# Performance work log

Measured on AMD Instinct MI355X. Metric: run time of the kernel, lower is better.

## Reference

```python
import jax, jax.numpy as jnp
import numpy as np

GROUP_SIZES = (64, 128, 256, 96, 160, 224, 192, 288, 320, 112, 80, 48, 32, 16, 32)
LENGTH = 512
ALPHABET = 21


def setup_inputs() -> dict:
    key = jax.random.key(0)
    keys = jax.random.split(key, len(GROUP_SIZES) + 1)
    n_samples = int(sum(GROUP_SIZES))
    inp = {"x": jax.random.normal(keys[0], (n_samples, LENGTH, ALPHABET), dtype=jnp.float32)}
    for i, g in enumerate(GROUP_SIZES):
        inp[f"mat{i}"] = jax.random.normal(keys[i + 1], (g, g), dtype=jnp.float32)
    return inp


def reference(x, mat0, mat1, mat2, mat3, mat4, mat5, mat6, mat7, mat8, mat9,
              mat10, mat11, mat12, mat13, mat14):
    mats = (mat0, mat1, mat2, mat3, mat4, mat5, mat6, mat7, mat8, mat9,
            mat10, mat11, mat12, mat13, mat14)
    # Block-diagonal grouped matmul along the sample dim: out[sl] = mats_i @ x[sl].
    # Group boundaries are static Python ints, so slicing is jit-friendly.
    pieces = []
    start = 0
    for m, g in zip(mats, GROUP_SIZES):
        xg = x[start:start + g]  # (g, L, A)
        pieces.append(jnp.einsum('gh,hla->gla', m, xg))
        start += g
    return jnp.concatenate(pieces, axis=0)
```

## Files before the change

kernel.cpp:

```cpp
#include <hip/hip_runtime.h>
#include <hip/hip_bf16.h>

#define NCOL 10752
#define NG 15
#define NTILES 23

typedef __bf16 bf16;
typedef __attribute__((ext_vector_type(8))) __bf16 bf16x8;
typedef __attribute__((ext_vector_type(4))) float f32x4;

__constant__ int c_gsize[NG]  = {64,128,256,96,160,224,192,288,320,112,80,48,32,16,32};
__constant__ int c_gstart[NG] = {0,64,192,448,544,704,928,1120,1408,1728,1840,1920,1968,2000,2016};
__constant__ int c_tgrp[NTILES] = {8,8,8,7,7,7,2,2,5,5,6,6,4,4,1,9,3,10,0,11,12,14,13};
__constant__ int c_trow[NTILES] = {0,128,256,0,128,256,0,128,0,128,0,128,0,128,0,0,0,0,0,0,0,0,0};

struct MatPtrs { const float* p[NG]; };

constexpr int BN = 128, BK = 32, BKp = 40;

__global__ __launch_bounds__(256)
void matapply_kernel(const float* __restrict__ x, MatPtrs mats, float* __restrict__ out)
{
    __shared__ bf16 sB[4][64][BKp];

    const int tid    = threadIdx.x;
    const int colb   = blockIdx.x * BN;
    const int tileid = blockIdx.y;

    const int grp  = c_tgrp[tileid];
    const int row0 = c_trow[tileid];
    const int g    = c_gsize[grp];
    const int s    = c_gstart[grp];
    const float* __restrict__ M = mats.p[grp];

    const int wave = tid >> 6;
    const int lane = tid & 63;
    const int wr   = (wave & 1) * 64;
    const int wc   = (wave >> 1) * 64;
    const int lm   = lane & 15;
    const int kq   = lane >> 4;
    const int kb   = kq * 8;

    bf16 (* __restrict__ sBw)[BKp] = sB[wave];

    const int nIter = (g + BK - 1) / BK;

    f32x4 acc[4][4];
    #pragma unroll
    for (int i = 0; i < 4; i++)
        #pragma unroll
        for (int j = 0; j < 4; j++)
            acc[i][j] = (f32x4){0.f, 0.f, 0.f, 0.f};

    int arow[4]; bool arok[4];
    #pragma unroll
    for (int i = 0; i < 4; i++) {
        arow[i] = row0 + wr + i * 16 + lm;
        arok[i] = arow[i] < g;
    }

    const float* xbase = x + (size_t)(s + kb) * NCOL + colb + wc + lm * 4;

    float4 a4[4][2];
    float4 xv[8];

    auto issueA = [&](int k0) {
        #pragma unroll
        for (int i = 0; i < 4; i++) {
            a4[i][0] = make_float4(0.f, 0.f, 0.f, 0.f);
            a4[i][1] = make_float4(0.f, 0.f, 0.f, 0.f);
            if (arok[i] && (k0 + kb) < g) {
                const float* p = M + (size_t)arow[i] * g + k0 + kb;
                a4[i][0] = *(const float4*)p;
                a4[i][1] = *(const float4*)(p + 4);
            }
        }
    };
    auto issueX = [&](int k0) {
        const float* p = xbase + (size_t)k0 * NCOL;
        #pragma unroll
        for (int q = 0; q < 8; q++)
            xv[q] = *(const float4*)(p + (size_t)q * NCOL);
    };

    issueA(0);
    issueX(0);

    for (int it = 0; it < nIter; ++it) {
        const int k0n = (it + 1) * BK;

        bf16x8 af[4];
        #pragma unroll
        for (int i = 0; i < 4; i++) {
            #pragma unroll
            for (int e = 0; e < 4; e++) {
                af[i][e]     = (bf16)(((const float*)&a4[i][0])[e]);
                af[i][4 + e] = (bf16)(((const float*)&a4[i][1])[e]);
            }
        }
        if (k0n < g) issueA(k0n);

        #pragma unroll
        for (int cc = 0; cc < 4; cc++) {
            const int lc = lm * 4 + cc;
            bf16x8 w;
            #pragma unroll
            for (int q = 0; q < 8; q++)
                w[q] = (bf16)(((const float*)&xv[q])[cc]);
            *(bf16x8*)&sBw[lc][kb ^ (((lc >> 3) & 3) << 3)] = w;
        }
        if (k0n < g) issueX(k0n);

        bf16x8 bfr[4];
        #pragma unroll
        for (int j = 0; j < 4; j++) {
            const int lc = j * 16 + lm;
            bfr[j] = *(const bf16x8*)&sBw[lc][kb ^ (((lc >> 3) & 3) << 3)];
        }
        #pragma unroll
        for (int i = 0; i < 4; i++)
            #pragma unroll
            for (int j = 0; j < 4; j++)
                acc[i][j] = __builtin_amdgcn_mfma_f32_16x16x32_bf16(af[i], bfr[j], acc[i][j], 0, 0, 0);
    }

    #pragma unroll
    for (int i = 0; i < 4; i++) {
        #pragma unroll
        for (int r = 0; r < 4; r++) {
            int row = row0 + wr + i * 16 + kq * 4 + r;
            if (row < g) {
                float* orow = out + (size_t)(s + row) * NCOL + colb + wc;
                #pragma unroll
                for (int j = 0; j < 4; j++)
                    orow[j * 16 + lm] = acc[i][j][r];
            }
        }
    }
}

extern "C" void kernel_launch(void* const* d_in, const int* in_sizes, int n_in,
                              void* d_out, int out_size, void* d_ws, size_t ws_size,
                              hipStream_t stream)
{
    const float* x = (const float*)d_in[0];
    MatPtrs mp;
    for (int i = 0; i < NG; i++) mp.p[i] = (const float*)d_in[1 + i];
    float* out = (float*)d_out;

    dim3 grid(NCOL / BN, NTILES);
    dim3 block(256);
    matapply_kernel<<<grid, block, 0, stream>>>(x, mp, out);
}
```

Baseline: 209.6 us.

## Switch to 64x256 block tiles with shared, double-buffered X staging

Each block now covers 64 rows by 256 columns instead of 128 by 128, and the row split is finer, giving 37 row tiles per column strip. All four waves load and convert one shared X tile, held in a double-buffered LDS array with a barrier per K step. Before, each wave staged its own private slice. The aim is less wasted row padding in odd-sized groups, better balance across tiles, and overlap of the next X load with the MFMAs. In exchange, each X column strip is now read by more row tiles, and block-wide synchronisation is added.

```diff
diff --git a/kernel.cpp b/kernel.cpp
--- a/kernel.cpp
+++ b/kernel.cpp
@@ -3,25 +3,26 @@
 
 #define NCOL 10752
 #define NG 15
-#define NTILES 23
+#define NTILES 37
 
 typedef __bf16 bf16;
 typedef __attribute__((ext_vector_type(8))) __bf16 bf16x8;
+typedef __attribute__((ext_vector_type(4))) __bf16 bf16x4;
 typedef __attribute__((ext_vector_type(4))) float f32x4;
 
 __constant__ int c_gsize[NG]  = {64,128,256,96,160,224,192,288,320,112,80,48,32,16,32};
 __constant__ int c_gstart[NG] = {0,64,192,448,544,704,928,1120,1408,1728,1840,1920,1968,2000,2016};
-__constant__ int c_tgrp[NTILES] = {8,8,8,7,7,7,2,2,5,5,6,6,4,4,1,9,3,10,0,11,12,14,13};
-__constant__ int c_trow[NTILES] = {0,128,256,0,128,256,0,128,0,128,0,128,0,128,0,0,0,0,0,0,0,0,0};
+__constant__ int c_tgrp[NTILES] = {8,8,8,8,8, 7,7,7,7,7, 2,2,2,2, 5,5,5,5, 6,6,6, 4,4,4, 1,1, 9,9, 3,3, 10,10, 0, 11, 12, 14, 13};
+__constant__ int c_trow[NTILES] = {0,64,128,192,256, 0,64,128,192,256, 0,64,128,192, 0,64,128,192, 0,64,128, 0,64,128, 0,64, 0,64, 0,64, 0,64, 0, 0, 0, 0, 0};
 
 struct MatPtrs { const float* p[NG]; };
 
-constexpr int BN = 128, BK = 32, BKp = 40;
+constexpr int BM = 64, BN = 256, BK = 32, BKp = 40;
 
 __global__ __launch_bounds__(256)
 void matapply_kernel(const float* __restrict__ x, MatPtrs mats, float* __restrict__ out)
 {
-    __shared__ bf16 sB[4][64][BKp];
+    __shared__ bf16 sB[2][BN][BKp];
 
     const int tid    = threadIdx.x;
     const int colb   = blockIdx.x * BN;
@@ -35,13 +36,12 @@
 
     const int wave = tid >> 6;
     const int lane = tid & 63;
-    const int wr   = (wave & 1) * 64;
-    const int wc   = (wave >> 1) * 64;
+    const int wc   = wave * 64;
     const int lm   = lane & 15;
     const int kq   = lane >> 4;
     const int kb   = kq * 8;
 
-    bf16 (* __restrict__ sBw)[BKp] = sB[wave];
+    const int xC = (tid & 63) * 4;
 
     const int nIter = (g + BK - 1) / BK;
 
@@ -55,11 +55,9 @@
     int arow[4]; bool arok[4];
     #pragma unroll
     for (int i = 0; i < 4; i++) {
-        arow[i] = row0 + wr + i * 16 + lm;
+        arow[i] = row0 + i * 16 + lm;
         arok[i] = arow[i] < g;
     }
-
-    const float* xbase = x + (size_t)(s + kb) * NCOL + colb + wc + lm * 4;
 
     float4 a4[4][2];
     float4 xv[8];
@@ -77,16 +75,37 @@
         }
     };
     auto issueX = [&](int k0) {
-        const float* p = xbase + (size_t)k0 * NCOL;
+        const float* p = x + (size_t)(s + k0 + 4 * wave) * NCOL + colb + xC;
         #pragma unroll
-        for (int q = 0; q < 8; q++)
-            xv[q] = *(const float4*)(p + (size_t)q * NCOL);
+        for (int t = 0; t < 2; t++)
+            #pragma unroll
+            for (int j = 0; j < 4; j++)
+                xv[t * 4 + j] = *(const float4*)(p + (size_t)(16 * t + j) * NCOL);
+    };
+    auto stageX = [&](int buf) {
+        #pragma unroll
+        for (int cc = 0; cc < 4; cc++) {
+            const int lc = xC + cc;
+            const int sw = ((lc >> 3) & 3) << 3;
+            #pragma unroll
+            for (int t = 0; t < 2; t++) {
+                bf16x4 w;
+                #pragma unroll
+                for (int j = 0; j < 4; j++)
+                    w[j] = (bf16)(((const float*)&xv[t * 4 + j])[cc]);
+                *(bf16x4*)&sB[buf][lc][(4 * wave + 16 * t) ^ sw] = w;
+            }
+        }
     };
 
     issueA(0);
     issueX(0);
+    stageX(0);
+    __syncthreads();
 
     for (int it = 0; it < nIter; ++it) {
+        const int cur = it & 1;
+        const bool more = (it + 1) < nIter;
         const int k0n = (it + 1) * BK;
 
         bf16x8 af[4];
@@ -98,37 +117,32 @@
                 af[i][4 + e] = (bf16)(((const float*)&a4[i][1])[e]);
             }
         }
-        if (k0n < g) issueA(k0n);
-
-        #pragma unroll
-        for (int cc = 0; cc < 4; cc++) {
-            const int lc = lm * 4 + cc;
-            bf16x8 w;
-            #pragma unroll
-            for (int q = 0; q < 8; q++)
-                w[q] = (bf16)(((const float*)&xv[q])[cc]);
-            *(bf16x8*)&sBw[lc][kb ^ (((lc >> 3) & 3) << 3)] = w;
-        }
-        if (k0n < g) issueX(k0n);
+        if (more) issueA(k0n);
+        if (more) issueX(k0n);
 
         bf16x8 bfr[4];
         #pragma unroll
         for (int j = 0; j < 4; j++) {
-            const int lc = j * 16 + lm;
-            bfr[j] = *(const bf16x8*)&sBw[lc][kb ^ (((lc >> 3) & 3) << 3)];
+            const int lc = wc + j * 16 + lm;
+            bfr[j] = *(const bf16x8*)&sB[cur][lc][kb ^ (((lc >> 3) & 3) << 3)];
         }
         #pragma unroll
         for (int i = 0; i < 4; i++)
             #pragma unroll
             for (int j = 0; j < 4; j++)
                 acc[i][j] = __builtin_amdgcn_mfma_f32_16x16x32_bf16(af[i], bfr[j], acc[i][j], 0, 0, 0);
+
+        if (more) {
+            stageX(1 - cur);
+            __syncthreads();
+        }
     }
 
     #pragma unroll
     for (int i = 0; i < 4; i++) {
         #pragma unroll
         for (int r = 0; r < 4; r++) {
-            int row = row0 + wr + i * 16 + kq * 4 + r;
+            int row = row0 + i * 16 + kq * 4 + r;
             if (row < g) {
                 float* orow = out + (size_t)(s + row) * NCOL + colb + wc;
                 #pragma unroll
```

New measurement: 213.2 us. Within noise of the previous version (+1.7%).
